# Kernel tuning notes

Hardware: AMD Instinct MI355X
Metric: run time of the kernel (lower is better)

Reference implementation:

```python
import jax, jax.numpy as jnp
import numpy as np

B, S, D = 2, 2048, 1280
H = 20
HD = D // H  # 64, rotary dim


def setup_inputs() -> dict:
    key = jax.random.key(0)
    ks = jax.random.split(key, 4)
    scale = 0.02
    return {
        "hidden_states": jax.random.normal(ks[0], (B, S, D), jnp.float32),
        "Wq": jax.random.normal(ks[1], (D, D), jnp.float32) * scale,
        "bq": jnp.zeros((D,), jnp.float32),
        "Wk": jax.random.normal(ks[2], (D, D), jnp.float32) * scale,
        "bk": jnp.zeros((D,), jnp.float32),
        "Wv": jax.random.normal(ks[3], (D, D), jnp.float32) * scale,
        "bv": jnp.zeros((D,), jnp.float32),
    }


def _rotate_half(x):
    x1, x2 = jnp.split(x, 2, axis=-1)
    return jnp.concatenate((-x2, x1), axis=-1)


def _rotary_cos_sin(seq_len, dim, dtype):
    inv_freq = 1.0 / (10000.0 ** (jnp.arange(0, dim, 2, dtype=jnp.float32) / dim))
    t = jnp.arange(seq_len, dtype=jnp.float32)
    freqs = jnp.einsum("i,j->ij", t, inv_freq)          # [S, dim/2]
    emb = jnp.concatenate((freqs, freqs), axis=-1)        # [S, dim]
    return jnp.cos(emb).astype(dtype)[None, None], jnp.sin(emb).astype(dtype)[None, None]


def reference(hidden_states, Wq, bq, Wk, bk, Wv, bv):
    b, s, d = hidden_states.shape
    # QKV projections, split heads -> [B, H, S, HD]
    def proj(W, bias):
        y = hidden_states @ W + bias
        return y.reshape(b, s, H, HD).transpose(0, 2, 1, 3)

    q = proj(Wq, bq) * (HD ** -0.5)  # scale BEFORE rotary, as in source
    k = proj(Wk, bk)
    v = proj(Wv, bv)

    cos, sin = _rotary_cos_sin(s, HD, q.dtype)
    q = q * cos + _rotate_half(q) * sin
    k = k * cos + _rotate_half(k) * sin

    scores = jnp.einsum("bhqd,bhkd->bhqk", q, k)
    probs = jax.nn.softmax(scores, axis=-1)
    ctx = jnp.einsum("bhqk,bhkd->bhqd", probs, v)
    return ctx.transpose(0, 2, 1, 3).reshape(b, s, d)
```

## Files before the change

kernel.cpp:

```cpp
#include <hip/hip_runtime.h>

#define DD 1280
#define SS 2048
#define HH 20

typedef __bf16 bf16x8 __attribute__((ext_vector_type(8)));
typedef float f32x4 __attribute__((ext_vector_type(4)));

typedef __attribute__((address_space(3))) unsigned int lds_uint;
typedef __attribute__((address_space(1))) unsigned int glb_uint;
#define GLL16(g, l) __builtin_amdgcn_global_load_lds((const glb_uint*)(g), (lds_uint*)(l), 16, 0, 0)

__device__ __forceinline__ unsigned short f2bf(float f) {
  union { float f; unsigned u; } v; v.f = f;
  unsigned r = v.u + 0x7fffu + ((v.u >> 16) & 1u);
  return (unsigned short)(r >> 16);
}
__device__ __forceinline__ unsigned f2u(float f) {
  union { float f; unsigned u; } v; v.f = f; return v.u;
}

__global__ __launch_bounds__(256) void prep_kernel(
    const float* __restrict__ X, const float* __restrict__ Wq,
    const float* __restrict__ Wk, const float* __restrict__ Wv,
    unsigned short* __restrict__ Xb, unsigned short* __restrict__ WT,
    float2* __restrict__ cs) {
  __shared__ unsigned short tile[32][33];
  int bid = blockIdx.x, tid = threadIdx.x;
  if (bid < 2560) {
    size_t base = (size_t)bid * 2048 + (size_t)tid * 8;
    const float4* xin = (const float4*)(X + base);
    float4 a = xin[0], c = xin[1];
    ushort4 o0 = make_ushort4(f2bf(a.x), f2bf(a.y), f2bf(a.z), f2bf(a.w));
    ushort4 o1 = make_ushort4(f2bf(c.x), f2bf(c.y), f2bf(c.z), f2bf(c.w));
    *(ushort4*)(Xb + base) = o0;
    *(ushort4*)(Xb + base + 4) = o1;
  } else if (bid < 7360) {
    int wb = bid - 2560;
    int mat = wb / 1600;
    int t = wb % 1600;
    int tn = t % 40, tk = t / 40;
    const float* W = (mat == 0) ? Wq : ((mat == 1) ? Wk : Wv);
    int k0 = tk * 32, n0 = tn * 32;
    int tc = tid & 31, tr = tid >> 5;
#pragma unroll
    for (int i = 0; i < 4; i++) {
      int kl = tr + i * 8;
      tile[kl][tc] = f2bf(W[(size_t)(k0 + kl) * DD + n0 + tc]);
    }
    __syncthreads();
    unsigned short* out = WT + (size_t)mat * DD * DD;
#pragma unroll
    for (int i = 0; i < 4; i++) {
      int nl = tr + i * 8;
      out[(size_t)(n0 + nl) * DD + k0 + tc] = tile[tc][nl];
    }
  } else {
    int idx = (bid - 7360) * 256 + tid;
    int sp = idx >> 5, j = idx & 31;
    float invf = exp2f(-(float)j * 0.41524101186092034f);
    float ang = (float)sp * invf;
    cs[idx] = make_float2(cosf(ang), sinf(ang));
  }
}

__global__ __launch_bounds__(256) void qkv_gemm_kernel(
    const unsigned short* __restrict__ Xb, const unsigned short* __restrict__ WT,
    const float* __restrict__ bq, const float* __restrict__ bk, const float* __restrict__ bv,
    const float2* __restrict__ cs,
    unsigned short* __restrict__ Qr, unsigned short* __restrict__ Kr,
    unsigned short* __restrict__ VT) {
  __shared__ __align__(16) unsigned short As[128 * 32];
  __shared__ __align__(16) unsigned short Bs[128 * 32];
  int bx = blockIdx.x;
  int mat = bx / 320;
  int r0 = bx % 320;
  int tm = r0 / 10, tn = r0 % 10;
  int m0 = tm * 128, n0 = tn * 128;
  int tid = threadIdx.x;
  int lane = tid & 63, wave = tid >> 6;
  int c15 = lane & 15, quad = lane >> 4;
  int wm = wave >> 1, wn = wave & 1;
  const unsigned short* Wm = WT + (size_t)mat * DD * DD;

  int rowA = tid >> 2;
  int c8 = (tid & 3) * 8;
  const unsigned short* gA0 = Xb + (size_t)(m0 + rowA) * DD + c8;
  const unsigned short* gA1 = gA0 + (size_t)64 * DD;
  const unsigned short* gB0 = Wm + (size_t)(n0 + rowA) * DD + c8;
  const unsigned short* gB1 = gB0 + (size_t)64 * DD;
  unsigned short* ldsA0 = As + wave * 512;
  unsigned short* ldsA1 = As + 2048 + wave * 512;
  unsigned short* ldsB0 = Bs + wave * 512;
  unsigned short* ldsB1 = Bs + 2048 + wave * 512;

  f32x4 acc[4][4] = {};

  for (int kk = 0; kk < DD; kk += 32) {
    __syncthreads();
    GLL16(gA0 + kk, ldsA0);
    GLL16(gA1 + kk, ldsA1);
    GLL16(gB0 + kk, ldsB0);
    GLL16(gB1 + kk, ldsB1);
    __syncthreads();
    bf16x8 af[4];
#pragma unroll
    for (int mi = 0; mi < 4; mi++)
      af[mi] = *(const bf16x8*)(As + (wm * 64 + mi * 16 + c15) * 32 + quad * 8);
#pragma unroll
    for (int ni = 0; ni < 4; ni++) {
      bf16x8 bfr = *(const bf16x8*)(Bs + (wn * 64 + ni * 16 + c15) * 32 + quad * 8);
#pragma unroll
      for (int mi = 0; mi < 4; mi++)
        acc[mi][ni] = __builtin_amdgcn_mfma_f32_16x16x32_bf16(af[mi], bfr, acc[mi][ni], 0, 0, 0);
    }
  }

  int growb = m0 + wm * 64;
  int gcolb = n0 + wn * 64;
  if (mat == 2) {
#pragma unroll
    for (int mi = 0; mi < 4; mi++) {
      int row0 = growb + mi * 16 + quad * 4;
      int bb_ = row0 >> 11, sp = row0 & 2047;
#pragma unroll
      for (int ni = 0; ni < 4; ni++) {
        int gcol = gcolb + ni * 16 + c15;
        float bias = bv[gcol];
        int hh = gcol >> 6, dd = gcol & 63;
        f32x4 v = acc[mi][ni];
        ushort4 o = make_ushort4(f2bf(v[0] + bias), f2bf(v[1] + bias),
                                 f2bf(v[2] + bias), f2bf(v[3] + bias));
        *(ushort4*)(VT + ((size_t)((bb_ * HH + hh) * 64 + dd)) * SS + sp) = o;
      }
    }
  } else {
    unsigned short* Out = (mat == 0) ? Qr : Kr;
    const float* bias = (mat == 0) ? bq : bk;
    float qs = (mat == 0) ? 0.18033688011112042f : 1.0f;
#pragma unroll
    for (int mi = 0; mi < 4; mi++) {
      int row0 = growb + mi * 16 + quad * 4;
#pragma unroll
      for (int ni = 0; ni < 2; ni++) {
        int gcol_lo = gcolb + ni * 16 + c15;
        int gcol_hi = gcol_lo + 32;
        float blo = bias[gcol_lo], bhi = bias[gcol_hi];
        int d = ni * 16 + c15;
        f32x4 lo = acc[mi][ni], hi = acc[mi][ni + 2];
#pragma unroll
        for (int r = 0; r < 4; r++) {
          int grow = row0 + r;
          float2 cv = cs[(size_t)(grow & 2047) * 32 + d];
          float xl = (lo[r] + blo) * qs, xh = (hi[r] + bhi) * qs;
          Out[(size_t)grow * DD + gcol_lo] = f2bf(xl * cv.x - xh * cv.y);
          Out[(size_t)grow * DD + gcol_hi] = f2bf(xh * cv.x + xl * cv.y);
        }
      }
    }
  }
}

__global__ __launch_bounds__(256)
__attribute__((amdgpu_waves_per_eu(2, 4)))
void attn_kernel(
    const unsigned short* __restrict__ Qr, const unsigned short* __restrict__ Kr,
    const unsigned short* __restrict__ VT, float* __restrict__ out) {
  __shared__ __align__(16) unsigned short Pall[4 * 64 * 64];
  __shared__ float Lbuf[64];
  int bx = blockIdx.x;
  int bh = bx % 40, qt = bx / 40;
  int b = bh / HH, h = bh % HH;
  int tid = threadIdx.x;
  int lane = tid & 63, w = tid >> 6;
  int c15 = lane & 15, quad = lane >> 4;
  int q0 = qt * 64;

  const unsigned short* Qbase = Qr + (size_t)(b * SS + q0) * DD + h * 64;
  bf16x8 qf[4][2];
#pragma unroll
  for (int mi = 0; mi < 4; mi++)
#pragma unroll
    for (int kc = 0; kc < 2; kc++)
      qf[mi][kc] = *(const bf16x8*)(Qbase + (size_t)(mi * 16 + c15) * DD + kc * 32 + quad * 8);

  const unsigned short* Kbase = Kr + (size_t)(b * SS + w * 32) * DD + h * 64;
  const unsigned short* Vbase = VT + (size_t)(bh * 64) * SS + w * 32;
  unsigned short* Pw = Pall + w * 4096;

  bf16x8 ones;
#pragma unroll
  for (int i = 0; i < 8; i++) ones[i] = (__bf16)1.0f;

  f32x4 of[4][4] = {};
  f32x4 ol[4] = {};

  for (int t = 0; t < 16; t++) {
    const unsigned short* Kt = Kbase + (size_t)(t * 128) * DD;
    const unsigned short* Vt = Vbase + t * 128;
    bf16x8 kf[2][2], vf[4];
#pragma unroll
    for (int ni = 0; ni < 2; ni++)
#pragma unroll
      for (int kc = 0; kc < 2; kc++)
        kf[ni][kc] = *(const bf16x8*)(Kt + (size_t)(ni * 16 + c15) * DD + kc * 32 + quad * 8);
#pragma unroll
    for (int nio = 0; nio < 4; nio++)
      vf[nio] = *(const bf16x8*)(Vt + (size_t)(nio * 16 + c15) * SS + quad * 8);

    f32x4 sc[4][2] = {};
#pragma unroll
    for (int ni = 0; ni < 2; ni++)
#pragma unroll
      for (int kc = 0; kc < 2; kc++)
#pragma unroll
        for (int mi = 0; mi < 4; mi++)
          sc[mi][ni] = __builtin_amdgcn_mfma_f32_16x16x32_bf16(qf[mi][kc], kf[ni][kc], sc[mi][ni], 0, 0, 0);

#pragma unroll
    for (int mi = 0; mi < 4; mi++)
#pragma unroll
      for (int ni = 0; ni < 2; ni++) {
        int kc8 = ni * 2 + (c15 >> 3);
#pragma unroll
        for (int r = 0; r < 4; r++) {
          unsigned u = f2u(__builtin_amdgcn_exp2f(sc[mi][ni][r]));
          int q = mi * 16 + quad * 4 + r;
          int pos = (kc8 + 2 * quad + r) & 7;
          Pw[q * 64 + pos * 8 + (c15 & 7)] = (unsigned short)(u >> 16);
        }
      }

#pragma unroll
    for (int mi = 0; mi < 4; mi++) {
      int pos = (quad + 2 * ((c15 >> 2) & 3) + (c15 & 3)) & 7;
      bf16x8 pf = *(const bf16x8*)(Pw + (mi * 16 + c15) * 64 + pos * 8);
#pragma unroll
      for (int nio = 0; nio < 4; nio++)
        of[mi][nio] = __builtin_amdgcn_mfma_f32_16x16x32_bf16(pf, vf[nio], of[mi][nio], 0, 0, 0);
      ol[mi] = __builtin_amdgcn_mfma_f32_16x16x32_bf16(pf, ones, ol[mi], 0, 0, 0);
    }
  }

  __syncthreads();
  float* Obuf = (float*)Pall;

  for (int pass = 0; pass < 4; pass++) {
    if (w == pass) {
#pragma unroll
      for (int mi = 0; mi < 4; mi++)
#pragma unroll
        for (int nio = 0; nio < 4; nio++)
#pragma unroll
          for (int r = 0; r < 4; r++) {
            int q = mi * 16 + quad * 4 + r;
            int d = nio * 16 + c15;
            if (pass == 0) Obuf[q * 65 + d] = of[mi][nio][r];
            else           Obuf[q * 65 + d] += of[mi][nio][r];
          }
      if (c15 == 0) {
#pragma unroll
        for (int mi = 0; mi < 4; mi++)
#pragma unroll
          for (int r = 0; r < 4; r++) {
            int q = mi * 16 + quad * 4 + r;
            if (pass == 0) Lbuf[q] = ol[mi][r];
            else           Lbuf[q] += ol[mi][r];
          }
      }
    }
    __syncthreads();
  }

  {
    int row = w * 16 + (lane >> 2);
    int col0 = (lane & 3) * 16;
    float invl = 1.0f / Lbuf[row];
    float* op = out + (size_t)(b * SS + q0 + row) * DD + h * 64 + col0;
    const float* ob = Obuf + row * 65 + col0;
#pragma unroll
    for (int j = 0; j < 4; j++) {
      float4 v = make_float4(ob[j * 4 + 0] * invl, ob[j * 4 + 1] * invl,
                             ob[j * 4 + 2] * invl, ob[j * 4 + 3] * invl);
      *(float4*)(op + j * 4) = v;
    }
  }
}

extern "C" void kernel_launch(void* const* d_in, const int* in_sizes, int n_in,
                              void* d_out, int out_size, void* d_ws, size_t ws_size,
                              hipStream_t stream) {
  (void)in_sizes; (void)n_in; (void)out_size; (void)ws_size;
  const float* X  = (const float*)d_in[0];
  const float* Wq = (const float*)d_in[1];
  const float* bq = (const float*)d_in[2];
  const float* Wk = (const float*)d_in[3];
  const float* bk = (const float*)d_in[4];
  const float* Wv = (const float*)d_in[5];
  const float* bv = (const float*)d_in[6];
  char* ws = (char*)d_ws;
  unsigned short* Xb  = (unsigned short*)(ws);
  unsigned short* WT  = (unsigned short*)(ws + 10485760);
  unsigned short* Qr  = (unsigned short*)(ws + 20316160);
  unsigned short* Kr  = (unsigned short*)(ws + 30801920);
  unsigned short* VTt = (unsigned short*)(ws + 41287680);
  float2* cstab       = (float2*)(ws + 51773440);
  hipLaunchKernelGGL(prep_kernel, dim3(7616), dim3(256), 0, stream, X, Wq, Wk, Wv, Xb, WT, cstab);
  hipLaunchKernelGGL(qkv_gemm_kernel, dim3(960), dim3(256), 0, stream, Xb, WT, bq, bk, bv, cstab, Qr, Kr, VTt);
  hipLaunchKernelGGL(attn_kernel, dim3(1280), dim3(256), 0, stream, Qr, Kr, VTt, (float*)d_out);
}
```

Baseline: 265.2 us.

## Keep P in registers via transposed QK MFMA and double-buffer K/V fragments

Computes scores as K·Q^T so each lane's exp2 results already form the A-operand layout of a 16x16x16 bf16 MFMA, removing the LDS round-trip for the P matrix. It also prefetches the next tile's K and V fragments into a second register buffer while the current tile is computed. The trade is twice as many smaller P·V MFMAs and higher register pressure from the double buffer, which could lower occupancy.

```diff
diff --git a/kernel.cpp b/kernel.cpp
--- a/kernel.cpp
+++ b/kernel.cpp
@@ -6,6 +6,7 @@
 
 typedef __bf16 bf16x8 __attribute__((ext_vector_type(8)));
 typedef float f32x4 __attribute__((ext_vector_type(4)));
+typedef short s16x4 __attribute__((ext_vector_type(4)));
 
 typedef __attribute__((address_space(3))) unsigned int lds_uint;
 typedef __attribute__((address_space(1))) unsigned int glb_uint;
@@ -161,12 +162,58 @@
   }
 }
 
+__device__ __forceinline__ void attn_load_frags(
+    bf16x8 (&kf)[2][2], s16x4 (&vf)[4][2],
+    const unsigned short* Kt, const unsigned short* Vt, int c15, int quad) {
+#pragma unroll
+  for (int ni = 0; ni < 2; ni++)
+#pragma unroll
+    for (int kc = 0; kc < 2; kc++)
+      kf[ni][kc] = *(const bf16x8*)(Kt + (size_t)(ni * 16 + c15) * DD + kc * 32 + quad * 8);
+#pragma unroll
+  for (int nio = 0; nio < 4; nio++)
+#pragma unroll
+    for (int ki = 0; ki < 2; ki++)
+      vf[nio][ki] = *(const s16x4*)(Vt + (size_t)(nio * 16 + c15) * SS + ki * 16 + quad * 4);
+}
+
+__device__ __forceinline__ void attn_tile(
+    const bf16x8 (&qf)[4][2], const bf16x8 (&kf)[2][2], const s16x4 (&vf)[4][2],
+    const s16x4& ones, f32x4 (&of)[4][4], f32x4 (&ol)[4]) {
+  f32x4 sc[2][4] = {};
+#pragma unroll
+  for (int ki = 0; ki < 2; ki++)
+#pragma unroll
+    for (int kc = 0; kc < 2; kc++)
+#pragma unroll
+      for (int mi = 0; mi < 4; mi++)
+        sc[ki][mi] = __builtin_amdgcn_mfma_f32_16x16x32_bf16(kf[ki][kc], qf[mi][kc], sc[ki][mi], 0, 0, 0);
+
+#pragma unroll
+  for (int ki = 0; ki < 2; ki++)
+#pragma unroll
+    for (int mi = 0; mi < 4; mi++) {
+      unsigned u0 = f2u(__builtin_amdgcn_exp2f(sc[ki][mi][0]));
+      unsigned u1 = f2u(__builtin_amdgcn_exp2f(sc[ki][mi][1]));
+      unsigned u2 = f2u(__builtin_amdgcn_exp2f(sc[ki][mi][2]));
+      unsigned u3 = f2u(__builtin_amdgcn_exp2f(sc[ki][mi][3]));
+      union { uint2 u; s16x4 s; } cv;
+      cv.u.x = (u0 >> 16) | (u1 & 0xffff0000u);
+      cv.u.y = (u2 >> 16) | (u3 & 0xffff0000u);
+      s16x4 pf = cv.s;
+#pragma unroll
+      for (int nio = 0; nio < 4; nio++)
+        of[mi][nio] = __builtin_amdgcn_mfma_f32_16x16x16bf16_1k(pf, vf[nio][ki], of[mi][nio], 0, 0, 0);
+      ol[mi] = __builtin_amdgcn_mfma_f32_16x16x16bf16_1k(pf, ones, ol[mi], 0, 0, 0);
+    }
+}
+
 __global__ __launch_bounds__(256)
 __attribute__((amdgpu_waves_per_eu(2, 4)))
 void attn_kernel(
     const unsigned short* __restrict__ Qr, const unsigned short* __restrict__ Kr,
     const unsigned short* __restrict__ VT, float* __restrict__ out) {
-  __shared__ __align__(16) unsigned short Pall[4 * 64 * 64];
+  __shared__ float Obuf[64 * 65];
   __shared__ float Lbuf[64];
   int bx = blockIdx.x;
   int bh = bx % 40, qt = bx / 40;
@@ -186,64 +233,31 @@
 
   const unsigned short* Kbase = Kr + (size_t)(b * SS + w * 32) * DD + h * 64;
   const unsigned short* Vbase = VT + (size_t)(bh * 64) * SS + w * 32;
-  unsigned short* Pw = Pall + w * 4096;
-
-  bf16x8 ones;
-#pragma unroll
-  for (int i = 0; i < 8; i++) ones[i] = (__bf16)1.0f;
+
+  s16x4 ones;
+#pragma unroll
+  for (int i = 0; i < 4; i++) ones[i] = (short)0x3F80;
 
   f32x4 of[4][4] = {};
   f32x4 ol[4] = {};
 
-  for (int t = 0; t < 16; t++) {
-    const unsigned short* Kt = Kbase + (size_t)(t * 128) * DD;
-    const unsigned short* Vt = Vbase + t * 128;
-    bf16x8 kf[2][2], vf[4];
-#pragma unroll
-    for (int ni = 0; ni < 2; ni++)
-#pragma unroll
-      for (int kc = 0; kc < 2; kc++)
-        kf[ni][kc] = *(const bf16x8*)(Kt + (size_t)(ni * 16 + c15) * DD + kc * 32 + quad * 8);
-#pragma unroll
-    for (int nio = 0; nio < 4; nio++)
-      vf[nio] = *(const bf16x8*)(Vt + (size_t)(nio * 16 + c15) * SS + quad * 8);
-
-    f32x4 sc[4][2] = {};
-#pragma unroll
-    for (int ni = 0; ni < 2; ni++)
-#pragma unroll
-      for (int kc = 0; kc < 2; kc++)
-#pragma unroll
-        for (int mi = 0; mi < 4; mi++)
-          sc[mi][ni] = __builtin_amdgcn_mfma_f32_16x16x32_bf16(qf[mi][kc], kf[ni][kc], sc[mi][ni], 0, 0, 0);
-
-#pragma unroll
-    for (int mi = 0; mi < 4; mi++)
-#pragma unroll
-      for (int ni = 0; ni < 2; ni++) {
-        int kc8 = ni * 2 + (c15 >> 3);
-#pragma unroll
-        for (int r = 0; r < 4; r++) {
-          unsigned u = f2u(__builtin_amdgcn_exp2f(sc[mi][ni][r]));
-          int q = mi * 16 + quad * 4 + r;
-          int pos = (kc8 + 2 * quad + r) & 7;
-          Pw[q * 64 + pos * 8 + (c15 & 7)] = (unsigned short)(u >> 16);
-        }
-      }
-
-#pragma unroll
-    for (int mi = 0; mi < 4; mi++) {
-      int pos = (quad + 2 * ((c15 >> 2) & 3) + (c15 & 3)) & 7;
-      bf16x8 pf = *(const bf16x8*)(Pw + (mi * 16 + c15) * 64 + pos * 8);
-#pragma unroll
-      for (int nio = 0; nio < 4; nio++)
-        of[mi][nio] = __builtin_amdgcn_mfma_f32_16x16x32_bf16(pf, vf[nio], of[mi][nio], 0, 0, 0);
-      ol[mi] = __builtin_amdgcn_mfma_f32_16x16x32_bf16(pf, ones, ol[mi], 0, 0, 0);
-    }
+  bf16x8 kfb[2][2][2];
+  s16x4 vfb[2][4][2];
+  attn_load_frags(kfb[0], vfb[0], Kbase, Vbase, c15, quad);
+
+  for (int t = 0; t < 16; t += 2) {
+    attn_load_frags(kfb[1], vfb[1],
+                    Kbase + (size_t)((t + 1) * 128) * DD, Vbase + (t + 1) * 128,
+                    c15, quad);
+    attn_tile(qf, kfb[0], vfb[0], ones, of, ol);
+    if (t + 2 < 16)
+      attn_load_frags(kfb[0], vfb[0],
+                      Kbase + (size_t)((t + 2) * 128) * DD, Vbase + (t + 2) * 128,
+                      c15, quad);
+    attn_tile(qf, kfb[1], vfb[1], ones, of, ol);
   }
 
   __syncthreads();
-  float* Obuf = (float*)Pall;
 
   for (int pass = 0; pass < 4; pass++) {
     if (w == pass) {
```

New measurement: 282.8 us. 1.07x slower.
